# Performance work log

Measured on AMD Instinct MI355X. Metric: run time of the kernel, lower is better.

Reference implementation:

```python
import jax, jax.numpy as jnp
import numpy as np


def setup_inputs() -> dict:
    key = jax.random.key(0)
    ks = jax.random.split(key, 8)
    B, C, H, W = 32, 98, 128, 128
    F, D = 256, 128
    return {
        "hm": jax.random.normal(ks[0], (B, C, H, W), dtype=jnp.float32),
        "feat": jax.random.normal(ks[1], (B, F, H, W), dtype=jnp.float32),
        "W_embed": jax.random.normal(ks[2], (2 + 1 + F, D), dtype=jnp.float32) * 0.05,
        "b_embed": jax.random.normal(ks[3], (D,), dtype=jnp.float32) * 0.05,
        "A": jax.random.normal(ks[4], (C, C), dtype=jnp.float32) * 0.05,
        "W_gcn": jax.random.normal(ks[5], (D, D), dtype=jnp.float32) * 0.05,
        "W_out": jax.random.normal(ks[6], (D, 2), dtype=jnp.float32) * 0.05,
        "b_out": jax.random.normal(ks[7], (2,), dtype=jnp.float32) * 0.05,
    }


def reference(hm, feat, W_embed, b_embed, A, W_gcn, W_out, b_out):
    # hm: [B, C, H, W] per-landmark heatmaps; feat: [B, F, H, W] backbone features.
    B, C, H, W = hm.shape
    F = feat.shape[1]

    # decode_heatmap: per-(batch, landmark) argmax location over HxW (batched,
    # replacing the original per-sample Python loops).
    hm_flat = hm.reshape(B, C, H * W)
    idx = jnp.argmax(hm_flat, axis=-1)                      # [B, C] int
    ys = idx // W
    xs = idx % W

    # node confidences: hm[i, classIds, ys, xs] -> batched gather
    conf = jnp.take_along_axis(hm_flat, idx[:, :, None], axis=-1)[..., 0]  # [B, C]

    # pooling_feature: gather the F-dim feature vector at each landmark location
    feat_flat = feat.reshape(B, F, H * W)
    vis = jnp.take_along_axis(feat_flat, idx[:, None, :], axis=-1)  # [B, F, C]
    vis = jnp.transpose(vis, (0, 2, 1))                              # [B, C, F]

    # normalized positions: node_positions (x, y) / hm_size [h, w] (as in source)
    hm_size = jnp.array([H, W], dtype=hm.dtype)
    pos = jnp.stack([xs, ys], axis=-1).astype(hm.dtype) / hm_size    # [B, C, 2]

    # GCN over landmarks (batched instead of per-sample calls)
    node = jnp.concatenate([pos, conf[..., None], vis], axis=-1)     # [B, C, 2+1+F]
    h0 = jax.nn.relu(jnp.einsum("bcf,fd->bcd", node, W_embed) + b_embed)
    h1 = jax.nn.relu(jnp.einsum("ij,bjd,de->bie", A, h0, W_gcn))     # learned adjacency
    out = jnp.einsum("bcd,do->bco", h1, W_out) + b_out               # [B, C, 2]
    return hm, out
```

## Files before the change

kernel.cpp:

```cpp
#include <hip/hip_runtime.h>

#define HM_B 32
#define HM_C 98
#define HM_H 128
#define HM_W 128
#define HWSZ (HM_H * HM_W)
#define HALF (HWSZ / 2)
#define FDIM 256
#define DDIM 128
#define NODE_F (2 + 1 + FDIM)
#define NODE_P 260
#define BC (HM_B * HM_C)
#define HM_ELEMS ((size_t)BC * HWSZ)
#define LCHUNK 8
#define ICHUNK 7
#define NTHR 256

typedef float f32x4 __attribute__((ext_vector_type(4)));

__global__ __launch_bounds__(NTHR) void k1_copy_argmax(
    const float* __restrict__ hm, float* __restrict__ out_hm,
    float* __restrict__ pconf, int* __restrict__ pidx) {
    const int bid = blockIdx.x;
    const int row = bid >> 1;
    const int half = bid & 1;
    const int tid = threadIdx.x;
    const size_t base = (size_t)row * HWSZ + (size_t)half * HALF;
    const f32x4* __restrict__ src = (const f32x4*)(hm + base);
    f32x4* __restrict__ dst = (f32x4*)(out_hm + base);

    float bv = -INFINITY;
    int bi = 0;
    #pragma unroll
    for (int t = 0; t < HALF / 4 / NTHR; ++t) {
        const int p = t * NTHR + tid;
        const f32x4 v = src[p];
        dst[p] = v;
        const float m4 = fmaxf(fmaxf(v[0], v[1]), fmaxf(v[2], v[3]));
        if (m4 > bv) {
            const int gbase = half * HALF + p * 4;
            if (v[0] > bv) { bv = v[0]; bi = gbase; }
            if (v[1] > bv) { bv = v[1]; bi = gbase + 1; }
            if (v[2] > bv) { bv = v[2]; bi = gbase + 2; }
            if (v[3] > bv) { bv = v[3]; bi = gbase + 3; }
        }
    }

    #pragma unroll
    for (int s = 1; s < 64; s <<= 1) {
        const float ov = __shfl_xor(bv, s, 64);
        const int oi = __shfl_xor(bi, s, 64);
        if (ov > bv || (ov == bv && oi < bi)) { bv = ov; bi = oi; }
    }

    __shared__ float wv[NTHR / 64];
    __shared__ int wi[NTHR / 64];
    if ((tid & 63) == 0) { wv[tid >> 6] = bv; wi[tid >> 6] = bi; }
    __syncthreads();
    if (tid == 0) {
        float fv = wv[0]; int fi = wi[0];
        #pragma unroll
        for (int w = 1; w < NTHR / 64; ++w)
            if (wv[w] > fv || (wv[w] == fv && wi[w] < fi)) { fv = wv[w]; fi = wi[w]; }
        pconf[bid] = fv; pidx[bid] = fi;
    }
}

__global__ __launch_bounds__(NTHR) void k2_embed(
    const float* __restrict__ feat, const float* __restrict__ pconf,
    const int* __restrict__ pidx, const float* __restrict__ W_embed,
    const float* __restrict__ b_embed, float* __restrict__ h0_ws) {
    const int bc0 = blockIdx.x * LCHUNK;
    const int tid = threadIdx.x;
    __shared__ float node_s[LCHUNK][NODE_P];
    __shared__ int locs[LCHUNK];

    if (tid < LCHUNK) {
        const int row = bc0 + tid;
        const float v0 = pconf[2 * row];
        const float v1 = pconf[2 * row + 1];
        const int loc = (v1 > v0) ? pidx[2 * row + 1] : pidx[2 * row];
        locs[tid] = loc;
        node_s[tid][0] = (float)(loc % HM_W) * (1.0f / (float)HM_H);
        node_s[tid][1] = (float)(loc / HM_W) * (1.0f / (float)HM_W);
        node_s[tid][2] = fmaxf(v0, v1);
    }
    __syncthreads();

    #pragma unroll
    for (int l = 0; l < LCHUNK; ++l) {
        const int bcL = bc0 + l;
        const int bb = bcL / HM_C;
        node_s[l][3 + tid] = feat[((size_t)(bb * FDIM + tid)) * HWSZ + locs[l]];
    }
    __syncthreads();

    const int d = tid & (DDIM - 1);
    const int lbase = (tid >> 7) * 4;
    const float bias = b_embed[d];
    float a0 = bias, a1 = bias, a2 = bias, a3 = bias;
    for (int f = 0; f < NODE_F; ++f) {
        const float w = W_embed[f * DDIM + d];
        a0 = fmaf(node_s[lbase + 0][f], w, a0);
        a1 = fmaf(node_s[lbase + 1][f], w, a1);
        a2 = fmaf(node_s[lbase + 2][f], w, a2);
        a3 = fmaf(node_s[lbase + 3][f], w, a3);
    }
    h0_ws[(size_t)(bc0 + lbase + 0) * DDIM + d] = fmaxf(a0, 0.f);
    h0_ws[(size_t)(bc0 + lbase + 1) * DDIM + d] = fmaxf(a1, 0.f);
    h0_ws[(size_t)(bc0 + lbase + 2) * DDIM + d] = fmaxf(a2, 0.f);
    h0_ws[(size_t)(bc0 + lbase + 3) * DDIM + d] = fmaxf(a3, 0.f);
}

__global__ __launch_bounds__(DDIM) void k3_gcn(
    const float* __restrict__ A, const float* __restrict__ h0_ws,
    const float* __restrict__ W_gcn, const float* __restrict__ W_out,
    const float* __restrict__ b_out, float* __restrict__ out2) {
    const int b = blockIdx.x / (HM_C / ICHUNK);
    const int i0 = (blockIdx.x % (HM_C / ICHUNK)) * ICHUNK;
    const int tid = threadIdx.x;

    __shared__ float arow[ICHUNK * HM_C];
    __shared__ float tmp_s[ICHUNK * DDIM];
    __shared__ float h1_s[ICHUNK * DDIM];

    for (int k = tid; k < ICHUNK * HM_C; k += DDIM)
        arow[k] = A[(i0 + k / HM_C) * HM_C + (k % HM_C)];
    __syncthreads();

    {
        float acc[ICHUNK];
        #pragma unroll
        for (int i = 0; i < ICHUNK; ++i) acc[i] = 0.f;
        for (int j = 0; j < HM_C; ++j) {
            const float v = h0_ws[((size_t)b * HM_C + j) * DDIM + tid];
            #pragma unroll
            for (int i = 0; i < ICHUNK; ++i)
                acc[i] = fmaf(arow[i * HM_C + j], v, acc[i]);
        }
        #pragma unroll
        for (int i = 0; i < ICHUNK; ++i) tmp_s[i * DDIM + tid] = acc[i];
    }
    __syncthreads();

    {
        float acc[ICHUNK];
        #pragma unroll
        for (int i = 0; i < ICHUNK; ++i) acc[i] = 0.f;
        for (int k = 0; k < DDIM; ++k) {
            const float w = W_gcn[k * DDIM + tid];
            #pragma unroll
            for (int i = 0; i < ICHUNK; ++i)
                acc[i] = fmaf(tmp_s[i * DDIM + k], w, acc[i]);
        }
        #pragma unroll
        for (int i = 0; i < ICHUNK; ++i) h1_s[i * DDIM + tid] = fmaxf(acc[i], 0.f);
    }
    __syncthreads();

    if (tid < ICHUNK * 2) {
        const int i = tid >> 1;
        const int o = tid & 1;
        float acc = b_out[o];
        for (int dd = 0; dd < DDIM; ++dd)
            acc = fmaf(h1_s[i * DDIM + dd], W_out[dd * 2 + o], acc);
        out2[((size_t)b * HM_C + i0 + i) * 2 + o] = acc;
    }
}

extern "C" void kernel_launch(void* const* d_in, const int* in_sizes, int n_in,
                              void* d_out, int out_size, void* d_ws, size_t ws_size,
                              hipStream_t stream) {
    const float* hm      = (const float*)d_in[0];
    const float* feat    = (const float*)d_in[1];
    const float* W_embed = (const float*)d_in[2];
    const float* b_embed = (const float*)d_in[3];
    const float* A       = (const float*)d_in[4];
    const float* W_gcn   = (const float*)d_in[5];
    const float* W_out   = (const float*)d_in[6];
    const float* b_out   = (const float*)d_in[7];

    float* out_hm = (float*)d_out;
    float* out2   = (float*)d_out + HM_ELEMS;

    char* ws = (char*)d_ws;
    float* pconf = (float*)ws;  ws += 2 * BC * sizeof(float);
    int*   pidx  = (int*)ws;    ws += 2 * BC * sizeof(int);
    float* h0_ws = (float*)ws;

    k1_copy_argmax<<<2 * BC, NTHR, 0, stream>>>(hm, out_hm, pconf, pidx);
    k2_embed<<<BC / LCHUNK, NTHR, 0, stream>>>(feat, pconf, pidx,
                                               W_embed, b_embed, h0_ws);
    k3_gcn<<<HM_B * (HM_C / ICHUNK), DDIM, 0, stream>>>(A, h0_ws, W_gcn,
                                                        W_out, b_out, out2);
}
```

Before: 135.4 us.

## Process full heatmap rows per block with software-pipelined loads and nontemporal stores

The copy-and-argmax kernel now has one block per heatmap row instead of two half-row blocks. Loads are software-pipelined in groups of four vectors, and the output copy uses nontemporal stores. The LDS cross-wave reduction and its barrier are dropped: each wave writes its partial argmax, and the embed kernel merges the four partials. The feature gather also becomes batched nontemporal loads. Fewer blocks means fewer waves in flight per row, while more loads are kept outstanding per thread.

New measurement: 109.6 us. 19.1% less time.

```diff
diff --git a/kernel.cpp b/kernel.cpp
--- a/kernel.cpp
+++ b/kernel.cpp
@@ -5,7 +5,6 @@
 #define HM_H 128
 #define HM_W 128
 #define HWSZ (HM_H * HM_W)
-#define HALF (HWSZ / 2)
 #define FDIM 256
 #define DDIM 128
 #define NODE_F (2 + 1 + FDIM)
@@ -15,35 +14,48 @@
 #define LCHUNK 8
 #define ICHUNK 7
 #define NTHR 256
+#define NWAVE (NTHR / 64)
 
 typedef float f32x4 __attribute__((ext_vector_type(4)));
 
 __global__ __launch_bounds__(NTHR) void k1_copy_argmax(
     const float* __restrict__ hm, float* __restrict__ out_hm,
     float* __restrict__ pconf, int* __restrict__ pidx) {
-    const int bid = blockIdx.x;
-    const int row = bid >> 1;
-    const int half = bid & 1;
+    const int row = blockIdx.x;
     const int tid = threadIdx.x;
-    const size_t base = (size_t)row * HWSZ + (size_t)half * HALF;
-    const f32x4* __restrict__ src = (const f32x4*)(hm + base);
-    f32x4* __restrict__ dst = (f32x4*)(out_hm + base);
+    const f32x4* __restrict__ src = (const f32x4*)(hm + (size_t)row * HWSZ);
+    f32x4* __restrict__ dst = (f32x4*)(out_hm + (size_t)row * HWSZ);
 
     float bv = -INFINITY;
     int bi = 0;
-    #pragma unroll
-    for (int t = 0; t < HALF / 4 / NTHR; ++t) {
-        const int p = t * NTHR + tid;
-        const f32x4 v = src[p];
-        dst[p] = v;
-        const float m4 = fmaxf(fmaxf(v[0], v[1]), fmaxf(v[2], v[3]));
-        if (m4 > bv) {
-            const int gbase = half * HALF + p * 4;
-            if (v[0] > bv) { bv = v[0]; bi = gbase; }
-            if (v[1] > bv) { bv = v[1]; bi = gbase + 1; }
-            if (v[2] > bv) { bv = v[2]; bi = gbase + 2; }
-            if (v[3] > bv) { bv = v[3]; bi = gbase + 3; }
-        }
+    f32x4 cur0 = src[0 * NTHR + tid];
+    f32x4 cur1 = src[1 * NTHR + tid];
+    f32x4 cur2 = src[2 * NTHR + tid];
+    f32x4 cur3 = src[3 * NTHR + tid];
+    #pragma unroll
+    for (int g = 0; g < 4; ++g) {
+        f32x4 nxt0, nxt1, nxt2, nxt3;
+        if (g < 3) {
+            nxt0 = src[((g + 1) * 4 + 0) * NTHR + tid];
+            nxt1 = src[((g + 1) * 4 + 1) * NTHR + tid];
+            nxt2 = src[((g + 1) * 4 + 2) * NTHR + tid];
+            nxt3 = src[((g + 1) * 4 + 3) * NTHR + tid];
+        }
+        #pragma unroll
+        for (int u = 0; u < 4; ++u) {
+            const f32x4 v = (u == 0) ? cur0 : (u == 1) ? cur1 : (u == 2) ? cur2 : cur3;
+            const int p = (g * 4 + u) * NTHR + tid;
+            __builtin_nontemporal_store(v, dst + p);
+            const float m4 = fmaxf(fmaxf(v[0], v[1]), fmaxf(v[2], v[3]));
+            if (m4 > bv) {
+                const int base = p * 4;
+                if (v[0] > bv) { bv = v[0]; bi = base; }
+                if (v[1] > bv) { bv = v[1]; bi = base + 1; }
+                if (v[2] > bv) { bv = v[2]; bi = base + 2; }
+                if (v[3] > bv) { bv = v[3]; bi = base + 3; }
+            }
+        }
+        cur0 = nxt0; cur1 = nxt1; cur2 = nxt2; cur3 = nxt3;
     }
 
     #pragma unroll
@@ -52,17 +64,9 @@
         const int oi = __shfl_xor(bi, s, 64);
         if (ov > bv || (ov == bv && oi < bi)) { bv = ov; bi = oi; }
     }
-
-    __shared__ float wv[NTHR / 64];
-    __shared__ int wi[NTHR / 64];
-    if ((tid & 63) == 0) { wv[tid >> 6] = bv; wi[tid >> 6] = bi; }
-    __syncthreads();
-    if (tid == 0) {
-        float fv = wv[0]; int fi = wi[0];
-        #pragma unroll
-        for (int w = 1; w < NTHR / 64; ++w)
-            if (wv[w] > fv || (wv[w] == fv && wi[w] < fi)) { fv = wv[w]; fi = wi[w]; }
-        pconf[bid] = fv; pidx[bid] = fi;
+    if ((tid & 63) == 0) {
+        pconf[row * NWAVE + (tid >> 6)] = bv;
+        pidx[row * NWAVE + (tid >> 6)] = bi;
     }
 }
 
@@ -77,22 +81,31 @@
 
     if (tid < LCHUNK) {
         const int row = bc0 + tid;
-        const float v0 = pconf[2 * row];
-        const float v1 = pconf[2 * row + 1];
-        const int loc = (v1 > v0) ? pidx[2 * row + 1] : pidx[2 * row];
-        locs[tid] = loc;
-        node_s[tid][0] = (float)(loc % HM_W) * (1.0f / (float)HM_H);
-        node_s[tid][1] = (float)(loc / HM_W) * (1.0f / (float)HM_W);
-        node_s[tid][2] = fmaxf(v0, v1);
-    }
-    __syncthreads();
-
+        float fv = pconf[row * NWAVE];
+        int fi = pidx[row * NWAVE];
+        #pragma unroll
+        for (int w = 1; w < NWAVE; ++w) {
+            const float ov = pconf[row * NWAVE + w];
+            const int oi = pidx[row * NWAVE + w];
+            if (ov > fv || (ov == fv && oi < fi)) { fv = ov; fi = oi; }
+        }
+        locs[tid] = fi;
+        node_s[tid][0] = (float)(fi % HM_W) * (1.0f / (float)HM_H);
+        node_s[tid][1] = (float)(fi / HM_W) * (1.0f / (float)HM_W);
+        node_s[tid][2] = fv;
+    }
+    __syncthreads();
+
+    float g[LCHUNK];
     #pragma unroll
     for (int l = 0; l < LCHUNK; ++l) {
-        const int bcL = bc0 + l;
-        const int bb = bcL / HM_C;
-        node_s[l][3 + tid] = feat[((size_t)(bb * FDIM + tid)) * HWSZ + locs[l]];
-    }
+        const int bb = (bc0 + l) / HM_C;
+        g[l] = __builtin_nontemporal_load(
+            feat + ((size_t)(bb * FDIM + tid)) * HWSZ + locs[l]);
+    }
+    #pragma unroll
+    for (int l = 0; l < LCHUNK; ++l)
+        node_s[l][3 + tid] = g[l];
     __syncthreads();
 
     const int d = tid & (DDIM - 1);
@@ -184,11 +197,11 @@
     float* out2   = (float*)d_out + HM_ELEMS;
 
     char* ws = (char*)d_ws;
-    float* pconf = (float*)ws;  ws += 2 * BC * sizeof(float);
-    int*   pidx  = (int*)ws;    ws += 2 * BC * sizeof(int);
+    float* pconf = (float*)ws;  ws += BC * NWAVE * sizeof(float);
+    int*   pidx  = (int*)ws;    ws += BC * NWAVE * sizeof(int);
     float* h0_ws = (float*)ws;
 
-    k1_copy_argmax<<<2 * BC, NTHR, 0, stream>>>(hm, out_hm, pconf, pidx);
+    k1_copy_argmax<<<BC, NTHR, 0, stream>>>(hm, out_hm, pconf, pidx);
     k2_embed<<<BC / LCHUNK, NTHR, 0, stream>>>(feat, pconf, pidx,
                                                W_embed, b_embed, h0_ws);
     k3_gcn<<<HM_B * (HM_C / ICHUNK), DDIM, 0, stream>>>(A, h0_ws, W_gcn,
```
